# Kernel tuning notes

Hardware: AMD Instinct MI355X
Metric: run time of the kernel (lower is better)

## Reference

```python
import jax, jax.numpy as jnp
import numpy as np

N_NODES = 100000
N_EDGES = 1600000
D_IN = 64
D_OUT = 64
K_ORDERS = 4  # K+1 Chebyshev orders (K=3)


def setup_inputs() -> dict:
    key = jax.random.key(0)
    k1, k2, k3, k4, k5 = jax.random.split(key, 5)
    x = jax.random.normal(k1, (N_NODES, D_IN), dtype=jnp.float32)
    edge_index = jax.random.randint(k2, (2, N_EDGES), 0, N_NODES, dtype=jnp.int64)
    edge_attr = jax.random.uniform(k3, (N_EDGES,), dtype=jnp.float32)
    weight = jax.random.normal(k4, (K_ORDERS, D_IN, D_OUT), dtype=jnp.float32) * 0.05
    bias = jax.random.normal(k5, (D_OUT,), dtype=jnp.float32) * 0.05
    return {"x": x, "edge_index": edge_index, "edge_attr": edge_attr,
            "weight": weight, "bias": bias}


def reference(x, edge_index, edge_attr, weight, bias):
    n = x.shape[0]
    row, col = edge_index[0], edge_index[1]
    # degree = number of edges per destination node (row)
    deg = jax.ops.segment_sum(jnp.ones_like(edge_attr), row, num_segments=n)
    dinv = jnp.where(deg > 0, deg ** -0.5, 0.0)
    # negative normalized adjacency acting as rescaled Laplacian
    lap = -dinv[row] * edge_attr * dinv[col]  # [E]

    def spmm(h):  # out[row] += lap * h[col]
        return jax.ops.segment_sum(lap[:, None] * h[col], row, num_segments=n)

    k_orders = weight.shape[0]
    tx0 = x
    out = tx0 @ weight[0]
    tx1 = spmm(tx0)
    out = out + tx1 @ weight[1]
    for k in range(2, k_orders):  # small fixed K, fine to unroll
        tx2 = 2.0 * spmm(tx1) - tx0
        out = out + tx2 @ weight[k]
        tx0, tx1 = tx1, tx2
    return out + bias
```

## Files before the change

### kernel.cpp

```cpp
#include <hip/hip_runtime.h>

#define D 64
#define BLK 256

#define NBSHIFT 9
#define NODES_PER_BKT 512
#define TA 4096

typedef unsigned int uint32;
typedef __attribute__((ext_vector_type(8))) short bf16x8;
typedef __attribute__((ext_vector_type(4))) float f32x4;

__device__ inline uint32 f2bf_u(float f) {
    uint32 u = __float_as_uint(f);
    u += 0x7FFFu + ((u >> 16) & 1u);
    return u >> 16;
}

__global__ void cvt_kernel(const float* __restrict__ x, uint2* __restrict__ xb, int n4) {
    int i = blockIdx.x * BLK + threadIdx.x;
    if (i < n4) {
        float4 v = ((const float4*)x)[i];
        uint2 pack;
        pack.x = f2bf_u(v.x) | (f2bf_u(v.y) << 16);
        pack.y = f2bf_u(v.z) | (f2bf_u(v.w) << 16);
        xb[i] = pack;
    }
}

__global__ void wf_kernel(const float* __restrict__ W, uint4* __restrict__ Wf) {
    int tid = blockIdx.x * 256 + threadIdx.x;
    int l = tid & 63;
    int g = tid >> 6;
    int kh = g & 1;
    int t = (g >> 1) & 3;
    int w = g >> 3;
    int n = t * 16 + (l & 15);
    int kbase = kh * 32 + (l >> 4) * 8;
    uint32 pk[4];
    #pragma unroll
    for (int i = 0; i < 4; ++i) {
        uint32 b0 = f2bf_u(W[(size_t)w * 4096 + (size_t)(kbase + 2 * i) * 64 + n]);
        uint32 b1 = f2bf_u(W[(size_t)w * 4096 + (size_t)(kbase + 2 * i + 1) * 64 + n]);
        pk[i] = b0 | (b1 << 16);
    }
    Wf[tid] = make_uint4(pk[0], pk[1], pk[2], pk[3]);
}

__global__ void hist_kernel(const int* __restrict__ row, uint32* __restrict__ bcount, int E) {
    __shared__ uint32 h[256];
    int tid = threadIdx.x;
    h[tid] = 0;
    __syncthreads();
    int base = blockIdx.x * TA;
    int end = min(base + TA, E);
    for (int e = base + tid; e < end; e += 256)
        atomicAdd(&h[(uint32)row[e] >> NBSHIFT], 1u);
    __syncthreads();
    if (h[tid]) atomicAdd(&bcount[tid], h[tid]);
}

__global__ void scan256_kernel(const uint32* __restrict__ bcount, uint32* __restrict__ gcursor,
                               uint32* __restrict__ bbase, int E) {
    __shared__ uint32 s[256];
    int tid = threadIdx.x;
    uint32 v = bcount[tid];
    s[tid] = v;
    __syncthreads();
    for (int off = 1; off < 256; off <<= 1) {
        uint32 t = (tid >= off) ? s[tid - off] : 0u;
        __syncthreads();
        s[tid] += t;
        __syncthreads();
    }
    uint32 excl = s[tid] - v;
    gcursor[tid] = excl;
    bbase[tid] = excl;
    if (tid == 255) bbase[256] = (uint32)E;
}

__global__ void binA_kernel(const int* __restrict__ row, const int* __restrict__ col,
                            const float* __restrict__ attr,
                            uint32* __restrict__ gcursor, int2* __restrict__ binned, int E) {
    __shared__ uint32 hist[256], baseg[256], lstart[256], lcur[256];
    __shared__ int2 stage[TA];
    __shared__ unsigned char sbkt[TA];
    int tid = threadIdx.x;
    int tile = blockIdx.x * TA;
    hist[tid] = 0;
    __syncthreads();

    uint32 px[16], py[16], bk[16];
    #pragma unroll
    for (int k = 0; k < 16; ++k) {
        int e = tile + k * 256 + tid;
        bk[k] = 0xFFFFFFFFu;
        if (e < E) {
            int r = row[e], c = col[e];
            uint32 b = (uint32)r >> NBSHIFT;
            bk[k] = b;
            px[k] = ((uint32)(r & (NODES_PER_BKT - 1)) << 17) | (uint32)c;
            py[k] = __float_as_uint(attr[e]);
            atomicAdd(&hist[b], 1u);
        }
    }
    __syncthreads();
    lcur[tid] = hist[tid];
    __syncthreads();
    for (int off = 1; off < 256; off <<= 1) {
        uint32 t = (tid >= off) ? lcur[tid - off] : 0u;
        __syncthreads();
        lcur[tid] += t;
        __syncthreads();
    }
    lstart[tid] = lcur[tid] - hist[tid];
    if (hist[tid] > 0) baseg[tid] = atomicAdd(&gcursor[tid], hist[tid]);
    lcur[tid] = lstart[tid];
    __syncthreads();
    #pragma unroll
    for (int k = 0; k < 16; ++k) {
        if (bk[k] != 0xFFFFFFFFu) {
            uint32 pos = atomicAdd(&lcur[bk[k]], 1u);
            stage[pos] = make_int2((int)px[k], (int)py[k]);
            sbkt[pos] = (unsigned char)bk[k];
        }
    }
    __syncthreads();
    int cnt = min(TA, E - tile);
    for (int i = tid; i < cnt; i += 256) {
        uint32 b = sbkt[i];
        uint32 dst = baseg[b] + (uint32)i - lstart[b];
        binned[dst] = stage[i];
    }
}

__global__ void binBdeg_kernel(const int2* __restrict__ binned, const uint32* __restrict__ bbase,
                               uint32* __restrict__ rowptr, float* __restrict__ dinv,
                               int N, int E) {
    __shared__ uint32 cnt[NODES_PER_BKT];
    __shared__ uint32 ps[256];
    int b = blockIdx.x;
    int tid = threadIdx.x;
    cnt[tid] = 0;
    cnt[tid + 256] = 0;
    __syncthreads();
    uint32 start = bbase[b], end = bbase[b + 1];
    for (uint32 i = start + tid; i < end; i += 256)
        atomicAdd(&cnt[(uint32)binned[i].x >> 17], 1u);
    __syncthreads();
    uint32 c0 = cnt[2 * tid], c1 = cnt[2 * tid + 1];
    ps[tid] = c0 + c1;
    __syncthreads();
    for (int off = 1; off < 256; off <<= 1) {
        uint32 t = (tid >= off) ? ps[tid - off] : 0u;
        __syncthreads();
        ps[tid] += t;
        __syncthreads();
    }
    uint32 pexcl = ps[tid] - (c0 + c1);
    int base = b << NBSHIFT;
    int n0 = base + 2 * tid, n1 = n0 + 1;
    if (n0 < N) {
        rowptr[n0] = start + pexcl;
        dinv[n0] = c0 ? rsqrtf((float)c0) : 0.0f;
    }
    if (n1 < N) {
        rowptr[n1] = start + pexcl + c0;
        dinv[n1] = c1 ? rsqrtf((float)c1) : 0.0f;
    }
    if (b == gridDim.x - 1 && tid == 0) rowptr[N] = (uint32)E;
}

__global__ void binBsort_kernel(const int2* __restrict__ binned, const uint32* __restrict__ bbase,
                                const uint32* __restrict__ rowptr, const float* __restrict__ dinv,
                                int2* __restrict__ pairs, int N) {
    __shared__ uint32 lcur[NODES_PER_BKT];
    __shared__ float ldin[NODES_PER_BKT];
    int b = blockIdx.x;
    int tid = threadIdx.x;
    int base = b << NBSHIFT;
    uint32 start = bbase[b], end = bbase[b + 1];
    for (int t = tid; t < NODES_PER_BKT; t += 256) {
        int node = base + t;
        lcur[t] = (node < N) ? (rowptr[node] - start) : 0u;
        ldin[t] = (node < N) ? dinv[node] : 0.0f;
    }
    __syncthreads();
    for (uint32 i = start + tid; i < end; i += 256) {
        int2 rec = binned[i];
        uint32 x = (uint32)rec.x;
        uint32 rl = x >> 17;
        uint32 c = x & 0x1FFFFu;
        float lap = -ldin[rl] * __int_as_float(rec.y) * dinv[c];
        uint32 pos = atomicAdd(&lcur[rl], 1u);
        pairs[start + pos] = make_int2((int)(c << 7), __float_as_int(lap));
    }
}

__global__ void spmm8_kernel(const uint32* __restrict__ rowptr, const int2* __restrict__ pairs,
                             const char* __restrict__ hb, const uint4* __restrict__ prev,
                             uint4* __restrict__ out, float scale, int N) {
    int n = blockIdx.x * 4 + (threadIdx.x >> 6);
    if (n >= N) return;
    int lane = threadIdx.x & 63;
    int q = lane >> 3;
    int sub = lane & 7;
    int off = sub * 16;
    uint32 j = rowptr[n];
    uint32 end = rowptr[n + 1];
    float a[8];
    #pragma unroll
    for (int i = 0; i < 8; ++i) a[i] = 0.0f;

    for (; j + 16 <= end; j += 16) {
        int2 m0 = pairs[j + q];
        int2 m1 = pairs[j + 8 + q];
        uint4 h0 = *(const uint4*)(hb + (uint32)m0.x + off);
        uint4 h1 = *(const uint4*)(hb + (uint32)m1.x + off);
        float l0 = __int_as_float(m0.y);
        float l1 = __int_as_float(m1.y);
        a[0] += l0 * __uint_as_float(h0.x << 16);
        a[1] += l0 * __uint_as_float(h0.x & 0xFFFF0000u);
        a[2] += l0 * __uint_as_float(h0.y << 16);
        a[3] += l0 * __uint_as_float(h0.y & 0xFFFF0000u);
        a[4] += l0 * __uint_as_float(h0.z << 16);
        a[5] += l0 * __uint_as_float(h0.z & 0xFFFF0000u);
        a[6] += l0 * __uint_as_float(h0.w << 16);
        a[7] += l0 * __uint_as_float(h0.w & 0xFFFF0000u);
        a[0] += l1 * __uint_as_float(h1.x << 16);
        a[1] += l1 * __uint_as_float(h1.x & 0xFFFF0000u);
        a[2] += l1 * __uint_as_float(h1.y << 16);
        a[3] += l1 * __uint_as_float(h1.y & 0xFFFF0000u);
        a[4] += l1 * __uint_as_float(h1.z << 16);
        a[5] += l1 * __uint_as_float(h1.z & 0xFFFF0000u);
        a[6] += l1 * __uint_as_float(h1.w << 16);
        a[7] += l1 * __uint_as_float(h1.w & 0xFFFF0000u);
    }
    for (; j < end; j += 8) {
        uint32 idx = j + q;
        bool act = idx < end;
        uint32 ci = act ? idx : (end - 1);
        int2 m = pairs[ci];
        float l = act ? __int_as_float(m.y) : 0.0f;
        uint4 h0 = *(const uint4*)(hb + (uint32)m.x + off);
        a[0] += l * __uint_as_float(h0.x << 16);
        a[1] += l * __uint_as_float(h0.x & 0xFFFF0000u);
        a[2] += l * __uint_as_float(h0.y << 16);
        a[3] += l * __uint_as_float(h0.y & 0xFFFF0000u);
        a[4] += l * __uint_as_float(h0.z << 16);
        a[5] += l * __uint_as_float(h0.z & 0xFFFF0000u);
        a[6] += l * __uint_as_float(h0.w << 16);
        a[7] += l * __uint_as_float(h0.w & 0xFFFF0000u);
    }
    #pragma unroll
    for (int i = 0; i < 8; ++i) {
        a[i] += __shfl_xor(a[i], 8);
        a[i] += __shfl_xor(a[i], 16);
        a[i] += __shfl_xor(a[i], 32);
    }

    if (q == 0) {
        float r[8];
        #pragma unroll
        for (int i = 0; i < 8; ++i) r[i] = scale * a[i];
        size_t slot = (size_t)n * 8 + sub;
        if (prev) {
            uint4 pv = prev[slot];
            r[0] -= __uint_as_float(pv.x << 16);
            r[1] -= __uint_as_float(pv.x & 0xFFFF0000u);
            r[2] -= __uint_as_float(pv.y << 16);
            r[3] -= __uint_as_float(pv.y & 0xFFFF0000u);
            r[4] -= __uint_as_float(pv.z << 16);
            r[5] -= __uint_as_float(pv.z & 0xFFFF0000u);
            r[6] -= __uint_as_float(pv.w << 16);
            r[7] -= __uint_as_float(pv.w & 0xFFFF0000u);
        }
        uint4 pack;
        pack.x = f2bf_u(r[0]) | (f2bf_u(r[1]) << 16);
        pack.y = f2bf_u(r[2]) | (f2bf_u(r[3]) << 16);
        pack.z = f2bf_u(r[4]) | (f2bf_u(r[5]) << 16);
        pack.w = f2bf_u(r[6]) | (f2bf_u(r[7]) << 16);
        out[slot] = pack;
    }
}

__global__ void gemm_mfma(const uint4* __restrict__ h0, const uint4* __restrict__ h1,
                          const uint4* __restrict__ h2, const uint4* __restrict__ h3,
                          const uint4* __restrict__ Wf, const float* __restrict__ bias,
                          float* __restrict__ out, int N) {
    int tid = threadIdx.x;
    int wave = tid >> 6;
    int lane = tid & 63;
    int quad = lane >> 4;
    int lo = lane & 15;
    int m0 = blockIdx.x * 64 + wave * 16;
    int mrow = m0 + lo;
    int mclamp = min(mrow, N - 1);

    f32x4 acc[4] = {{0.f,0.f,0.f,0.f},{0.f,0.f,0.f,0.f},{0.f,0.f,0.f,0.f},{0.f,0.f,0.f,0.f}};
    const uint4* hs[4] = { h0, h1, h2, h3 };
    #pragma unroll
    for (int w = 0; w < 4; ++w) {
        union { uint4 u; bf16x8 v; } a0, a1;
        a0.u = hs[w][(size_t)mclamp * 8 + quad];
        a1.u = hs[w][(size_t)mclamp * 8 + 4 + quad];
        #pragma unroll
        for (int t = 0; t < 4; ++t) {
            union { uint4 u; bf16x8 v; } b0, b1;
            b0.u = Wf[(w * 8 + t * 2 + 0) * 64 + lane];
            b1.u = Wf[(w * 8 + t * 2 + 1) * 64 + lane];
            acc[t] = __builtin_amdgcn_mfma_f32_16x16x32_bf16(a0.v, b0.v, acc[t], 0, 0, 0);
            acc[t] = __builtin_amdgcn_mfma_f32_16x16x32_bf16(a1.v, b1.v, acc[t], 0, 0, 0);
        }
    }
    #pragma unroll
    for (int t = 0; t < 4; ++t) {
        int col = t * 16 + lo;
        float bv = bias[col];
        #pragma unroll
        for (int r = 0; r < 4; ++r) {
            int rowi = m0 + quad * 4 + r;
            if (rowi < N) out[(size_t)rowi * 64 + col] = acc[t][r] + bv;
        }
    }
}

extern "C" void kernel_launch(void* const* d_in, const int* in_sizes, int n_in,
                              void* d_out, int out_size, void* d_ws, size_t ws_size,
                              hipStream_t stream) {
    const float* x    = (const float*)d_in[0];
    const int*   ei   = (const int*)d_in[1];
    const float* attr = (const float*)d_in[2];
    const float* W    = (const float*)d_in[3];
    const float* bias = (const float*)d_in[4];
    float* out = (float*)d_out;

    const int N = in_sizes[0] / D;
    const int E = in_sizes[1] / 2;
    const int* row = ei;
    const int* col = ei + E;
    const int NB = (N + NODES_PER_BKT - 1) >> NBSHIFT;

    char* p = (char*)d_ws;
    int2*     pairs   = (int2*)p;                p += (size_t)E * 8;
    uint2*    xb      = (uint2*)p;               p += (size_t)N * D * 2;
    uint2*    T1      = (uint2*)p;               p += (size_t)N * D * 2;
    uint2*    T2      = (uint2*)p;               p += (size_t)N * D * 2;
    uint2*    T3      = (uint2*)p;               p += (size_t)N * D * 2;
    uint4*    Wf      = (uint4*)p;               p += 2048 * 16;
    uint32*   rowptr  = (uint32*)p;              p += (size_t)(N + 1) * 4;
    uint32*   bcount  = (uint32*)p;              p += 256 * 4;
    uint32*   gcursor = (uint32*)p;              p += 256 * 4;
    uint32*   bbase   = (uint32*)p;              p += 257 * 4;
    float*    dinv    = (float*)p;
    int2*     binned  = (int2*)T3;

    const int gSp = (N + 3) / 4;
    const int gGm = (N + 63) / 64;
    const int gTile = (E + TA - 1) / TA;
    const int gCvt = ((N * D / 4) + BLK - 1) / BLK;

    hipMemsetAsync(bcount, 0, 256 * 4, stream);
    cvt_kernel<<<gCvt, BLK, 0, stream>>>(x, xb, N * D / 4);
    wf_kernel<<<8, 256, 0, stream>>>(W, Wf);
    hist_kernel<<<gTile, 256, 0, stream>>>(row, bcount, E);
    scan256_kernel<<<1, 256, 0, stream>>>(bcount, gcursor, bbase, E);
    binA_kernel<<<gTile, 256, 0, stream>>>(row, col, attr, gcursor, binned, E);
    binBdeg_kernel<<<NB, 256, 0, stream>>>(binned, bbase, rowptr, dinv, N, E);
    binBsort_kernel<<<NB, 256, 0, stream>>>(binned, bbase, rowptr, dinv, pairs, N);

    spmm8_kernel<<<gSp, BLK, 0, stream>>>(rowptr, pairs, (const char*)xb, nullptr, (uint4*)T1, 1.0f, N);
    spmm8_kernel<<<gSp, BLK, 0, stream>>>(rowptr, pairs, (const char*)T1, (const uint4*)xb, (uint4*)T2, 2.0f, N);
    spmm8_kernel<<<gSp, BLK, 0, stream>>>(rowptr, pairs, (const char*)T2, (const uint4*)T1, (uint4*)T3, 2.0f, N);
    gemm_mfma<<<gGm, BLK, 0, stream>>>((const uint4*)xb, (const uint4*)T1, (const uint4*)T2,
                                       (const uint4*)T3, Wf, bias, out, N);
}
```

Before: 313.4 us.

## Reassociate third Chebyshev order through weight and fuse preprocessing kernels

Rewrites the last order T3 = 2*L*T2 - T1 so that T2*W3 is computed in the GEMM and a final SpMM over the 64-wide projected result adds 2*L*(T2 W3) into the output, while T1's weight becomes W1-W3. The column scaling by dinv is moved out of the per-edge values and applied to the gathered features instead, which removes the per-edge dinv[col] gather in the sort pass. The histogram, x conversion and weight packing kernels are merged into one launch, and the degree and sort bin kernels are merged into one. This trades an extra bf16 rounding step and a read-modify-write of the fp32 output for removing one SpMM output buffer and its GEMM input stream.

```diff
diff --git a/kernel.cpp b/kernel.cpp
--- a/kernel.cpp
+++ b/kernel.cpp
@@ -17,47 +17,59 @@
     return u >> 16;
 }
 
-__global__ void cvt_kernel(const float* __restrict__ x, uint2* __restrict__ xb, int n4) {
-    int i = blockIdx.x * BLK + threadIdx.x;
-    if (i < n4) {
-        float4 v = ((const float4*)x)[i];
-        uint2 pack;
-        pack.x = f2bf_u(v.x) | (f2bf_u(v.y) << 16);
-        pack.y = f2bf_u(v.z) | (f2bf_u(v.w) << 16);
-        xb[i] = pack;
-    }
-}
-
-__global__ void wf_kernel(const float* __restrict__ W, uint4* __restrict__ Wf) {
-    int tid = blockIdx.x * 256 + threadIdx.x;
-    int l = tid & 63;
-    int g = tid >> 6;
-    int kh = g & 1;
-    int t = (g >> 1) & 3;
-    int w = g >> 3;
-    int n = t * 16 + (l & 15);
-    int kbase = kh * 32 + (l >> 4) * 8;
-    uint32 pk[4];
-    #pragma unroll
-    for (int i = 0; i < 4; ++i) {
-        uint32 b0 = f2bf_u(W[(size_t)w * 4096 + (size_t)(kbase + 2 * i) * 64 + n]);
-        uint32 b1 = f2bf_u(W[(size_t)w * 4096 + (size_t)(kbase + 2 * i + 1) * 64 + n]);
-        pk[i] = b0 | (b1 << 16);
-    }
-    Wf[tid] = make_uint4(pk[0], pk[1], pk[2], pk[3]);
-}
-
-__global__ void hist_kernel(const int* __restrict__ row, uint32* __restrict__ bcount, int E) {
-    __shared__ uint32 h[256];
+__global__ void prep_kernel(const int* __restrict__ row, uint32* __restrict__ bcount,
+                            const float* __restrict__ x, uint2* __restrict__ xb,
+                            const float* __restrict__ W, uint4* __restrict__ Wf,
+                            int E, int n4, int gTile, int gCvt) {
+    int bid = blockIdx.x;
     int tid = threadIdx.x;
-    h[tid] = 0;
-    __syncthreads();
-    int base = blockIdx.x * TA;
-    int end = min(base + TA, E);
-    for (int e = base + tid; e < end; e += 256)
-        atomicAdd(&h[(uint32)row[e] >> NBSHIFT], 1u);
-    __syncthreads();
-    if (h[tid]) atomicAdd(&bcount[tid], h[tid]);
+    if (bid < gTile) {
+        __shared__ uint32 h[256];
+        h[tid] = 0;
+        __syncthreads();
+        int base = bid * TA;
+        int end = min(base + TA, E);
+        for (int e = base + tid; e < end; e += 256)
+            atomicAdd(&h[(uint32)row[e] >> NBSHIFT], 1u);
+        __syncthreads();
+        if (h[tid]) atomicAdd(&bcount[tid], h[tid]);
+    } else if (bid < gTile + gCvt) {
+        int i = (bid - gTile) * 256 + tid;
+        if (i < n4) {
+            float4 v = ((const float4*)x)[i];
+            uint2 pack;
+            pack.x = f2bf_u(v.x) | (f2bf_u(v.y) << 16);
+            pack.y = f2bf_u(v.z) | (f2bf_u(v.w) << 16);
+            xb[i] = pack;
+        }
+    } else {
+        int t2 = (bid - gTile - gCvt) * 256 + tid;
+        int l = t2 & 63;
+        int g = t2 >> 6;
+        int kh = g & 1;
+        int t = (g >> 1) & 3;
+        int w = g >> 3;
+        int n = t * 16 + (l & 15);
+        int kbase = kh * 32 + (l >> 4) * 8;
+        uint32 pk[4];
+        #pragma unroll
+        for (int i = 0; i < 4; ++i) {
+            #pragma unroll
+            for (int h2 = 0; h2 < 1; ++h2) {}
+            int k0 = kbase + 2 * i, k1 = k0 + 1;
+            float v0, v1;
+            if (w == 1) {
+                v0 = W[4096 + (size_t)k0 * 64 + n] - W[3 * 4096 + (size_t)k0 * 64 + n];
+                v1 = W[4096 + (size_t)k1 * 64 + n] - W[3 * 4096 + (size_t)k1 * 64 + n];
+            } else {
+                int ws = (w == 0) ? 0 : (w == 2) ? 2 : 3;
+                v0 = W[(size_t)ws * 4096 + (size_t)k0 * 64 + n];
+                v1 = W[(size_t)ws * 4096 + (size_t)k1 * 64 + n];
+            }
+            pk[i] = f2bf_u(v0) | (f2bf_u(v1) << 16);
+        }
+        Wf[t2] = make_uint4(pk[0], pk[1], pk[2], pk[3]);
+    }
 }
 
 __global__ void scan256_kernel(const uint32* __restrict__ bcount, uint32* __restrict__ gcursor,
@@ -134,72 +146,76 @@
     }
 }
 
-__global__ void binBdeg_kernel(const int2* __restrict__ binned, const uint32* __restrict__ bbase,
-                               uint32* __restrict__ rowptr, float* __restrict__ dinv,
-                               int N, int E) {
+__global__ void binB_kernel(const int2* __restrict__ binned, const uint32* __restrict__ bbase,
+                            uint32* __restrict__ rowptr, float* __restrict__ dinv,
+                            int2* __restrict__ pairs,
+                            const uint2* __restrict__ xb, uint2* __restrict__ gx,
+                            int N, int E, int lastB) {
     __shared__ uint32 cnt[NODES_PER_BKT];
     __shared__ uint32 ps[256];
-    int b = blockIdx.x;
-    int tid = threadIdx.x;
-    cnt[tid] = 0;
-    cnt[tid + 256] = 0;
-    __syncthreads();
-    uint32 start = bbase[b], end = bbase[b + 1];
-    for (uint32 i = start + tid; i < end; i += 256)
-        atomicAdd(&cnt[(uint32)binned[i].x >> 17], 1u);
-    __syncthreads();
-    uint32 c0 = cnt[2 * tid], c1 = cnt[2 * tid + 1];
-    ps[tid] = c0 + c1;
-    __syncthreads();
-    for (int off = 1; off < 256; off <<= 1) {
-        uint32 t = (tid >= off) ? ps[tid - off] : 0u;
-        __syncthreads();
-        ps[tid] += t;
-        __syncthreads();
-    }
-    uint32 pexcl = ps[tid] - (c0 + c1);
-    int base = b << NBSHIFT;
-    int n0 = base + 2 * tid, n1 = n0 + 1;
-    if (n0 < N) {
-        rowptr[n0] = start + pexcl;
-        dinv[n0] = c0 ? rsqrtf((float)c0) : 0.0f;
-    }
-    if (n1 < N) {
-        rowptr[n1] = start + pexcl + c0;
-        dinv[n1] = c1 ? rsqrtf((float)c1) : 0.0f;
-    }
-    if (b == gridDim.x - 1 && tid == 0) rowptr[N] = (uint32)E;
-}
-
-__global__ void binBsort_kernel(const int2* __restrict__ binned, const uint32* __restrict__ bbase,
-                                const uint32* __restrict__ rowptr, const float* __restrict__ dinv,
-                                int2* __restrict__ pairs, int N) {
     __shared__ uint32 lcur[NODES_PER_BKT];
     __shared__ float ldin[NODES_PER_BKT];
     int b = blockIdx.x;
     int tid = threadIdx.x;
     int base = b << NBSHIFT;
     uint32 start = bbase[b], end = bbase[b + 1];
-    for (int t = tid; t < NODES_PER_BKT; t += 256) {
-        int node = base + t;
-        lcur[t] = (node < N) ? (rowptr[node] - start) : 0u;
-        ldin[t] = (node < N) ? dinv[node] : 0.0f;
-    }
+    cnt[tid] = 0;
+    cnt[tid + 256] = 0;
+    __syncthreads();
+    for (uint32 i = start + tid; i < end; i += 256)
+        atomicAdd(&cnt[(uint32)binned[i].x >> 17], 1u);
+    __syncthreads();
+    uint32 c0 = cnt[2 * tid], c1 = cnt[2 * tid + 1];
+    ps[tid] = c0 + c1;
+    __syncthreads();
+    for (int off = 1; off < 256; off <<= 1) {
+        uint32 t = (tid >= off) ? ps[tid - off] : 0u;
+        __syncthreads();
+        ps[tid] += t;
+        __syncthreads();
+    }
+    uint32 pexcl = ps[tid] - (c0 + c1);
+    float d0 = c0 ? rsqrtf((float)c0) : 0.0f;
+    float d1 = c1 ? rsqrtf((float)c1) : 0.0f;
+    lcur[2 * tid] = pexcl;
+    lcur[2 * tid + 1] = pexcl + c0;
+    ldin[2 * tid] = d0;
+    ldin[2 * tid + 1] = d1;
+    int n0 = base + 2 * tid, n1 = n0 + 1;
+    if (n0 < N) { rowptr[n0] = start + pexcl;      dinv[n0] = d0; }
+    if (n1 < N) { rowptr[n1] = start + pexcl + c0; dinv[n1] = d1; }
+    if (b == lastB && tid == 0) rowptr[N] = (uint32)E;
     __syncthreads();
     for (uint32 i = start + tid; i < end; i += 256) {
         int2 rec = binned[i];
-        uint32 x = (uint32)rec.x;
-        uint32 rl = x >> 17;
-        uint32 c = x & 0x1FFFFu;
-        float lap = -ldin[rl] * __int_as_float(rec.y) * dinv[c];
+        uint32 xx = (uint32)rec.x;
+        uint32 rl = xx >> 17;
+        uint32 c = xx & 0x1FFFFu;
+        float y = -ldin[rl] * __int_as_float(rec.y);
         uint32 pos = atomicAdd(&lcur[rl], 1u);
-        pairs[start + pos] = make_int2((int)(c << 7), __float_as_int(lap));
-    }
-}
-
-__global__ void spmm8_kernel(const uint32* __restrict__ rowptr, const int2* __restrict__ pairs,
-                             const char* __restrict__ hb, const uint4* __restrict__ prev,
-                             uint4* __restrict__ out, float scale, int N) {
+        pairs[start + pos] = make_int2((int)(c << 7), __float_as_int(y));
+    }
+    for (int i = tid; i < NODES_PER_BKT * 16; i += 256) {
+        int r = i >> 4;
+        int node = base + r;
+        if (node >= N) break;
+        uint2 v = xb[(size_t)node * 16 + (i & 15)];
+        float s = ldin[r];
+        float f0 = __uint_as_float(v.x << 16) * s;
+        float f1 = __uint_as_float(v.x & 0xFFFF0000u) * s;
+        float f2 = __uint_as_float(v.y << 16) * s;
+        float f3 = __uint_as_float(v.y & 0xFFFF0000u) * s;
+        uint2 o;
+        o.x = f2bf_u(f0) | (f2bf_u(f1) << 16);
+        o.y = f2bf_u(f2) | (f2bf_u(f3) << 16);
+        gx[(size_t)node * 16 + (i & 15)] = o;
+    }
+}
+
+__global__ void spmm_t_kernel(const uint32* __restrict__ rowptr, const int2* __restrict__ pairs,
+                              const char* __restrict__ gin, const uint4* __restrict__ prev,
+                              uint4* __restrict__ outT, uint4* __restrict__ outG,
+                              const float* __restrict__ dinv, float scale, int N) {
     int n = blockIdx.x * 4 + (threadIdx.x >> 6);
     if (n >= N) return;
     int lane = threadIdx.x & 63;
@@ -215,8 +231,8 @@
     for (; j + 16 <= end; j += 16) {
         int2 m0 = pairs[j + q];
         int2 m1 = pairs[j + 8 + q];
-        uint4 h0 = *(const uint4*)(hb + (uint32)m0.x + off);
-        uint4 h1 = *(const uint4*)(hb + (uint32)m1.x + off);
+        uint4 h0 = *(const uint4*)(gin + (uint32)m0.x + off);
+        uint4 h1 = *(const uint4*)(gin + (uint32)m1.x + off);
         float l0 = __int_as_float(m0.y);
         float l1 = __int_as_float(m1.y);
         a[0] += l0 * __uint_as_float(h0.x << 16);
@@ -242,7 +258,7 @@
         uint32 ci = act ? idx : (end - 1);
         int2 m = pairs[ci];
         float l = act ? __int_as_float(m.y) : 0.0f;
-        uint4 h0 = *(const uint4*)(hb + (uint32)m.x + off);
+        uint4 h0 = *(const uint4*)(gin + (uint32)m.x + off);
         a[0] += l * __uint_as_float(h0.x << 16);
         a[1] += l * __uint_as_float(h0.x & 0xFFFF0000u);
         a[2] += l * __uint_as_float(h0.y << 16);
@@ -280,14 +296,96 @@
         pack.y = f2bf_u(r[2]) | (f2bf_u(r[3]) << 16);
         pack.z = f2bf_u(r[4]) | (f2bf_u(r[5]) << 16);
         pack.w = f2bf_u(r[6]) | (f2bf_u(r[7]) << 16);
-        out[slot] = pack;
+        outT[slot] = pack;
+        if (outG) {
+            float dn = dinv[n];
+            uint4 pg;
+            pg.x = f2bf_u(r[0] * dn) | (f2bf_u(r[1] * dn) << 16);
+            pg.y = f2bf_u(r[2] * dn) | (f2bf_u(r[3] * dn) << 16);
+            pg.z = f2bf_u(r[4] * dn) | (f2bf_u(r[5] * dn) << 16);
+            pg.w = f2bf_u(r[6] * dn) | (f2bf_u(r[7] * dn) << 16);
+            outG[slot] = pg;
+        }
+    }
+}
+
+__global__ void spmm_f_kernel(const uint32* __restrict__ rowptr, const int2* __restrict__ pairs,
+                              const char* __restrict__ gin, float* __restrict__ out, int N) {
+    int n = blockIdx.x * 4 + (threadIdx.x >> 6);
+    if (n >= N) return;
+    int lane = threadIdx.x & 63;
+    int q = lane >> 3;
+    int sub = lane & 7;
+    int off = sub * 16;
+    uint32 j = rowptr[n];
+    uint32 end = rowptr[n + 1];
+    float a[8];
+    #pragma unroll
+    for (int i = 0; i < 8; ++i) a[i] = 0.0f;
+
+    for (; j + 16 <= end; j += 16) {
+        int2 m0 = pairs[j + q];
+        int2 m1 = pairs[j + 8 + q];
+        uint4 h0 = *(const uint4*)(gin + (uint32)m0.x + off);
+        uint4 h1 = *(const uint4*)(gin + (uint32)m1.x + off);
+        float l0 = __int_as_float(m0.y);
+        float l1 = __int_as_float(m1.y);
+        a[0] += l0 * __uint_as_float(h0.x << 16);
+        a[1] += l0 * __uint_as_float(h0.x & 0xFFFF0000u);
+        a[2] += l0 * __uint_as_float(h0.y << 16);
+        a[3] += l0 * __uint_as_float(h0.y & 0xFFFF0000u);
+        a[4] += l0 * __uint_as_float(h0.z << 16);
+        a[5] += l0 * __uint_as_float(h0.z & 0xFFFF0000u);
+        a[6] += l0 * __uint_as_float(h0.w << 16);
+        a[7] += l0 * __uint_as_float(h0.w & 0xFFFF0000u);
+        a[0] += l1 * __uint_as_float(h1.x << 16);
+        a[1] += l1 * __uint_as_float(h1.x & 0xFFFF0000u);
+        a[2] += l1 * __uint_as_float(h1.y << 16);
+        a[3] += l1 * __uint_as_float(h1.y & 0xFFFF0000u);
+        a[4] += l1 * __uint_as_float(h1.z << 16);
+        a[5] += l1 * __uint_as_float(h1.z & 0xFFFF0000u);
+        a[6] += l1 * __uint_as_float(h1.w << 16);
+        a[7] += l1 * __uint_as_float(h1.w & 0xFFFF0000u);
+    }
+    for (; j < end; j += 8) {
+        uint32 idx = j + q;
+        bool act = idx < end;
+        uint32 ci = act ? idx : (end - 1);
+        int2 m = pairs[ci];
+        float l = act ? __int_as_float(m.y) : 0.0f;
+        uint4 h0 = *(const uint4*)(gin + (uint32)m.x + off);
+        a[0] += l * __uint_as_float(h0.x << 16);
+        a[1] += l * __uint_as_float(h0.x & 0xFFFF0000u);
+        a[2] += l * __uint_as_float(h0.y << 16);
+        a[3] += l * __uint_as_float(h0.y & 0xFFFF0000u);
+        a[4] += l * __uint_as_float(h0.z << 16);
+        a[5] += l * __uint_as_float(h0.z & 0xFFFF0000u);
+        a[6] += l * __uint_as_float(h0.w << 16);
+        a[7] += l * __uint_as_float(h0.w & 0xFFFF0000u);
+    }
+    #pragma unroll
+    for (int i = 0; i < 8; ++i) {
+        a[i] += __shfl_xor(a[i], 8);
+        a[i] += __shfl_xor(a[i], 16);
+        a[i] += __shfl_xor(a[i], 32);
+    }
+
+    if (q == 0) {
+        float* basep = out + (size_t)n * 64 + sub * 8;
+        float4 o0 = *(float4*)basep;
+        float4 o1 = *(float4*)(basep + 4);
+        o0.x += 2.0f * a[0]; o0.y += 2.0f * a[1]; o0.z += 2.0f * a[2]; o0.w += 2.0f * a[3];
+        o1.x += 2.0f * a[4]; o1.y += 2.0f * a[5]; o1.z += 2.0f * a[6]; o1.w += 2.0f * a[7];
+        *(float4*)basep = o0;
+        *(float4*)(basep + 4) = o1;
     }
 }
 
 __global__ void gemm_mfma(const uint4* __restrict__ h0, const uint4* __restrict__ h1,
-                          const uint4* __restrict__ h2, const uint4* __restrict__ h3,
+                          const uint4* __restrict__ h2,
                           const uint4* __restrict__ Wf, const float* __restrict__ bias,
-                          float* __restrict__ out, int N) {
+                          const float* __restrict__ dinv,
+                          float* __restrict__ out, unsigned short* __restrict__ gU, int N) {
     int tid = threadIdx.x;
     int wave = tid >> 6;
     int lane = tid & 63;
@@ -298,9 +396,10 @@
     int mclamp = min(mrow, N - 1);
 
     f32x4 acc[4] = {{0.f,0.f,0.f,0.f},{0.f,0.f,0.f,0.f},{0.f,0.f,0.f,0.f},{0.f,0.f,0.f,0.f}};
-    const uint4* hs[4] = { h0, h1, h2, h3 };
-    #pragma unroll
-    for (int w = 0; w < 4; ++w) {
+    f32x4 accU[4] = {{0.f,0.f,0.f,0.f},{0.f,0.f,0.f,0.f},{0.f,0.f,0.f,0.f},{0.f,0.f,0.f,0.f}};
+    const uint4* hs[3] = { h0, h1, h2 };
+    #pragma unroll
+    for (int w = 0; w < 3; ++w) {
         union { uint4 u; bf16x8 v; } a0, a1;
         a0.u = hs[w][(size_t)mclamp * 8 + quad];
         a1.u = hs[w][(size_t)mclamp * 8 + 4 + quad];
@@ -312,6 +411,16 @@
             acc[t] = __builtin_amdgcn_mfma_f32_16x16x32_bf16(a0.v, b0.v, acc[t], 0, 0, 0);
             acc[t] = __builtin_amdgcn_mfma_f32_16x16x32_bf16(a1.v, b1.v, acc[t], 0, 0, 0);
         }
+        if (w == 2) {
+            #pragma unroll
+            for (int t = 0; t < 4; ++t) {
+                union { uint4 u; bf16x8 v; } b0, b1;
+                b0.u = Wf[(3 * 8 + t * 2 + 0) * 64 + lane];
+                b1.u = Wf[(3 * 8 + t * 2 + 1) * 64 + lane];
+                accU[t] = __builtin_amdgcn_mfma_f32_16x16x32_bf16(a0.v, b0.v, accU[t], 0, 0, 0);
+                accU[t] = __builtin_amdgcn_mfma_f32_16x16x32_bf16(a1.v, b1.v, accU[t], 0, 0, 0);
+            }
+        }
     }
     #pragma unroll
     for (int t = 0; t < 4; ++t) {
@@ -320,7 +429,11 @@
         #pragma unroll
         for (int r = 0; r < 4; ++r) {
             int rowi = m0 + quad * 4 + r;
-            if (rowi < N) out[(size_t)rowi * 64 + col] = acc[t][r] + bv;
+            if (rowi < N) {
+                out[(size_t)rowi * 64 + col] = acc[t][r] + bv;
+                float dn = dinv[rowi];
+                gU[(size_t)rowi * 64 + col] = (unsigned short)f2bf_u(accU[t][r] * dn);
+            }
         }
     }
 }
@@ -344,34 +457,36 @@
     char* p = (char*)d_ws;
     int2*     pairs   = (int2*)p;                p += (size_t)E * 8;
     uint2*    xb      = (uint2*)p;               p += (size_t)N * D * 2;
+    uint2*    gx      = (uint2*)p;               p += (size_t)N * D * 2;
+    uint2*    g1      = (uint2*)p;               p += (size_t)N * D * 2;
     uint2*    T1      = (uint2*)p;               p += (size_t)N * D * 2;
     uint2*    T2      = (uint2*)p;               p += (size_t)N * D * 2;
-    uint2*    T3      = (uint2*)p;               p += (size_t)N * D * 2;
     uint4*    Wf      = (uint4*)p;               p += 2048 * 16;
     uint32*   rowptr  = (uint32*)p;              p += (size_t)(N + 1) * 4;
     uint32*   bcount  = (uint32*)p;              p += 256 * 4;
     uint32*   gcursor = (uint32*)p;              p += 256 * 4;
     uint32*   bbase   = (uint32*)p;              p += 257 * 4;
     float*    dinv    = (float*)p;
-    int2*     binned  = (int2*)T3;
+    int2*     binned  = (int2*)T1;
+    uint2*    gU      = gx;
 
     const int gSp = (N + 3) / 4;
     const int gGm = (N + 63) / 64;
     const int gTile = (E + TA - 1) / TA;
-    const int gCvt = ((N * D / 4) + BLK - 1) / BLK;
+    const int gCvt = ((N * D / 4) + 255) / 256;
 
     hipMemsetAsync(bcount, 0, 256 * 4, stream);
-    cvt_kernel<<<gCvt, BLK, 0, stream>>>(x, xb, N * D / 4);
-    wf_kernel<<<8, 256, 0, stream>>>(W, Wf);
-    hist_kernel<<<gTile, 256, 0, stream>>>(row, bcount, E);
+    prep_kernel<<<gTile + gCvt + 8, 256, 0, stream>>>(row, bcount, x, xb, W, Wf,
+                                                      E, N * D / 4, gTile, gCvt);
     scan256_kernel<<<1, 256, 0, stream>>>(bcount, gcursor, bbase, E);
     binA_kernel<<<gTile, 256, 0, stream>>>(row, col, attr, gcursor, binned, E);
-    binBdeg_kernel<<<NB, 256, 0, stream>>>(binned, bbase, rowptr, dinv, N, E);
-    binBsort_kernel<<<NB, 256, 0, stream>>>(binned, bbase, rowptr, dinv, pairs, N);
-
-    spmm8_kernel<<<gSp, BLK, 0, stream>>>(rowptr, pairs, (const char*)xb, nullptr, (uint4*)T1, 1.0f, N);
-    spmm8_kernel<<<gSp, BLK, 0, stream>>>(rowptr, pairs, (const char*)T1, (const uint4*)xb, (uint4*)T2, 2.0f, N);
-    spmm8_kernel<<<gSp, BLK, 0, stream>>>(rowptr, pairs, (const char*)T2, (const uint4*)T1, (uint4*)T3, 2.0f, N);
+    binB_kernel<<<NB, 256, 0, stream>>>(binned, bbase, rowptr, dinv, pairs, xb, gx, N, E, NB - 1);
+
+    spmm_t_kernel<<<gSp, BLK, 0, stream>>>(rowptr, pairs, (const char*)gx, nullptr,
+                                           (uint4*)T1, (uint4*)g1, dinv, 1.0f, N);
+    spmm_t_kernel<<<gSp, BLK, 0, stream>>>(rowptr, pairs, (const char*)g1, (const uint4*)xb,
+                                           (uint4*)T2, nullptr, dinv, 2.0f, N);
     gemm_mfma<<<gGm, BLK, 0, stream>>>((const uint4*)xb, (const uint4*)T1, (const uint4*)T2,
-                                       (const uint4*)T3, Wf, bias, out, N);
-}
+                                       Wf, bias, dinv, out, (unsigned short*)gU, N);
+    spmm_f_kernel<<<gSp, BLK, 0, stream>>>(rowptr, pairs, (const char*)gU, out, N);
+}
```

Measured after the change: 320.2 us. +2.2%, slower.
